# Kernel optimization log

Hardware: AMD Instinct MI355X
Metric: run time of the kernel (lower is better)

## Reference

```python
import jax, jax.numpy as jnp
import numpy as np

B, T1, T2 = 16, 2048, 512
N_MEL, N_TEXT, N_ATT = 80, 256, 256
TEMPERATURE = 0.0005


def _conv1d(x, w, b):
    # x: (B, T, Cin), w: (K, Cin, Cout), 'same' padding
    pad = (w.shape[0] - 1) // 2
    y = jax.lax.conv_general_dilated(
        x, w, window_strides=(1,), padding=[(pad, pad)],
        dimension_numbers=("NWC", "WIO", "NWC"))
    return y + b


def setup_inputs() -> dict:
    key = jax.random.key(0)
    ks = jax.random.split(key, 16)
    s = 0.05
    queries = jax.random.normal(ks[0], (B, N_MEL, T1), jnp.float32)
    keys = jax.random.normal(ks[1], (B, T2, N_TEXT), jnp.float32)
    attn_prior = jax.random.uniform(ks[2], (B, T2, T1), jnp.float32)
    lengths = jax.random.randint(ks[3], (B,), T2 // 2, T2 + 1)
    mask = jnp.arange(T2)[None, :] >= lengths[:, None]  # True = padding
    # key_proj params: Conv(256->512,k3), ReLU, Conv(512->256,k1)
    kw1 = jax.random.normal(ks[4], (3, N_TEXT, 2 * N_TEXT), jnp.float32) * s
    kb1 = jnp.zeros((2 * N_TEXT,), jnp.float32)
    kw2 = jax.random.normal(ks[5], (1, 2 * N_TEXT, N_ATT), jnp.float32) * s
    kb2 = jnp.zeros((N_ATT,), jnp.float32)
    # query_proj params: Conv(80->160,k3), ReLU, Conv(160->80,k1), ReLU, Conv(80->256,k1)
    qw1 = jax.random.normal(ks[6], (3, N_MEL, 2 * N_MEL), jnp.float32) * s
    qb1 = jnp.zeros((2 * N_MEL,), jnp.float32)
    qw2 = jax.random.normal(ks[7], (1, 2 * N_MEL, N_MEL), jnp.float32) * s
    qb2 = jnp.zeros((N_MEL,), jnp.float32)
    qw3 = jax.random.normal(ks[8], (1, N_MEL, N_ATT), jnp.float32) * s
    qb3 = jnp.zeros((N_ATT,), jnp.float32)
    return dict(queries=queries, keys=keys, mask=mask, attn_prior=attn_prior,
                kw1=kw1, kb1=kb1, kw2=kw2, kb2=kb2,
                qw1=qw1, qb1=qb1, qw2=qw2, qb2=qb2, qw3=qw3, qb3=qb3)


def reference(queries, keys, mask, attn_prior,
              kw1, kb1, kw2, kb2, qw1, qb1, qw2, qb2, qw3, qb3):
    # keys: (B, T2, C_text) -> ke: (B, T2, n_att)
    ke = _conv1d(jax.nn.relu(_conv1d(keys, kw1, kb1)), kw2, kb2)
    # queries: (B, C_mel, T1) -> (B, T1, C_mel) -> qe: (B, T1, n_att)
    q = queries.transpose(0, 2, 1)
    q = jax.nn.relu(_conv1d(jax.nn.relu(_conv1d(q, qw1, qb1)), qw2, qb2))
    qe = _conv1d(q, qw3, qb3)
    # pairwise squared L2 distance over channels, via |q|^2 + |k|^2 - 2 q.k
    q2 = jnp.sum(qe * qe, axis=-1)            # (B, T1)
    k2 = jnp.sum(ke * ke, axis=-1)            # (B, T2)
    qk = jnp.einsum("btc,bsc->bts", qe, ke)   # (B, T1, T2)
    dist = q2[:, :, None] + k2[:, None, :] - 2.0 * qk
    attn = (-TEMPERATURE * dist)[:, None]      # (B, 1, T1, T2)
    # prior in log-space
    attn = jax.nn.log_softmax(attn, axis=3) + jnp.log(
        attn_prior.transpose(0, 2, 1)[:, None] + 1e-8)
    attn_logprob = attn
    attn = jnp.where(mask[:, None, None, :], -jnp.inf, attn)
    attn = jax.nn.softmax(attn, axis=3)
    return attn, attn_logprob
```

## Files before the change

### kernel.cpp

```cpp
#include <hip/hip_runtime.h>
#include <cmath>

#define NB    16
#define TT1   2048
#define TT2   512
#define NATT  256
#define TEMP  0.0005f

#define KP_SZ   (NB*514*256)
#define KE_SZ   (NB*512*256)
#define QP_SZ   (NB*2050*80)
#define QE_SZ   (NB*2048*256)
#define W1T_SZ  (512*768)
#define W2T_SZ  (256*512)
#define W3T_SZ  (160*256)
#define W4T_SZ  (80*160)
#define W5T_SZ  (256*96)
#define WTOT_SZ (W1T_SZ+W2T_SZ+W3T_SZ+W4T_SZ+W5T_SZ)
#define LGP_SZ  (NB*TT1*TT2)

#define PREP_PLT_BLK  ((TT1/64)*(TT2/64)*NB)
#define PREP_PK_BLK   (KP_SZ/256)
#define PREP_WT_BLK   (WTOT_SZ/256)
#define PREP_QT_BLK   (NB*(TT1/64))
#define CONV_KEY_BLK  (NB*512/32)
#define CONV_QRY_BLK  (NB*2048/128)

typedef __attribute__((ext_vector_type(8))) short short8v;
typedef __attribute__((ext_vector_type(4))) float f32x4;

__device__ inline ushort f2bf(float f) {
    unsigned int u = __float_as_uint(f);
    u += 0x7fff + ((u >> 16) & 1);
    return (ushort)(u >> 16);
}
__device__ inline float bf2f(ushort u) {
    return __uint_as_float(((unsigned int)u) << 16);
}


__global__ __launch_bounds__(256) void prep_kernel(
    const float* __restrict__ keys, ushort* __restrict__ kp,
    const float* __restrict__ kw1, const float* __restrict__ kw2,
    const float* __restrict__ qw1, const float* __restrict__ qw2,
    const float* __restrict__ qw3,
    ushort* __restrict__ w1t, ushort* __restrict__ w2t, ushort* __restrict__ w3t,
    ushort* __restrict__ w4t, ushort* __restrict__ w5t,
    const float* __restrict__ queries, ushort* __restrict__ qp,
    const float* __restrict__ prior, ushort* __restrict__ lgp)
{
    __shared__ float T[80][65];
    const int bx  = blockIdx.x;
    const int tid = threadIdx.x;

    if (bx < PREP_PLT_BLK) {
        const int l    = bx;
        const int t1_0 = (l & 31) * 64;
        const int t2_0 = ((l >> 5) & 7) * 64;
        const int b    = l >> 8;
        const int j4 = tid & 15;
        const int r0 = tid >> 4;
        #pragma unroll
        for (int p = 0; p < 4; ++p) {
            const f32x4 v = __builtin_nontemporal_load(
                (const f32x4*)(prior + ((size_t)b * TT2 + t2_0 + r0 + p * 16) * TT1
                                + t1_0 + j4 * 4));
            T[r0 + p * 16][j4 * 4 + 0] = v.x;
            T[r0 + p * 16][j4 * 4 + 1] = v.y;
            T[r0 + p * 16][j4 * 4 + 2] = v.z;
            T[r0 + p * 16][j4 * 4 + 3] = v.w;
        }
        __syncthreads();
        const int j  = tid & 63;
        const int i0 = (tid >> 6) * 16;
        #pragma unroll
        for (int r = 0; r < 16; ++r) {
            const int p = i0 + r;
            const float v = T[j][p];
            lgp[((size_t)b * TT1 + t1_0 + p) * TT2 + t2_0 + j] = f2bf(__logf(v + 1e-8f));
        }
        return;
    }
    if (bx < PREP_PLT_BLK + PREP_PK_BLK) {
        const int idx = (bx - PREP_PLT_BLK) * 256 + tid;
        int c = idx & 255;
        int r = (idx >> 8) % 514;
        int b = idx / (514 * 256);
        float v = 0.f;
        if (r >= 1 && r <= 512)
            v = keys[((size_t)b * 512 + (r - 1)) * 256 + c];
        kp[idx] = f2bf(v);
        return;
    }
    if (bx < PREP_PLT_BLK + PREP_PK_BLK + PREP_WT_BLK) {
        int idx = (bx - PREP_PLT_BLK - PREP_PK_BLK) * 256 + tid;
        const float* w; ushort* wt; int Kreal, Kpad, N;
        if (idx < W1T_SZ) {
            w = kw1; wt = w1t; Kreal = 768; Kpad = 768; N = 512;
        } else if ((idx -= W1T_SZ) < W2T_SZ) {
            w = kw2; wt = w2t; Kreal = 512; Kpad = 512; N = 256;
        } else if ((idx -= W2T_SZ) < W3T_SZ) {
            w = qw1; wt = w3t; Kreal = 240; Kpad = 256; N = 160;
        } else if ((idx -= W3T_SZ) < W4T_SZ) {
            w = qw2; wt = w4t; Kreal = 160; Kpad = 160; N = 80;
        } else {
            idx -= W4T_SZ;
            w = qw3; wt = w5t; Kreal = 80; Kpad = 96; N = 256;
        }
        int k = idx % Kpad;
        int n = idx / Kpad;
        wt[idx] = (k < Kreal) ? f2bf(w[(size_t)k * N + n]) : (ushort)0;
        return;
    }
    {
        const int l  = bx - PREP_PLT_BLK - PREP_PK_BLK - PREP_WT_BLK;
        const int b  = l >> 5;
        const int t0 = (l & 31) * 64;
        const int g  = tid >> 6;
        const int j  = tid & 63;
        #pragma unroll
        for (int r = 0; r < 20; ++r) {
            const int c = g * 20 + r;
            T[c][j] = queries[((size_t)b * 80 + c) * 2048 + t0 + j];
        }
        __syncthreads();
        const int tt = tid >> 2;
        const int c0 = (tid & 3) * 20;
        ushort* qrow = qp + (size_t)b * (2050 * 80) + (size_t)(t0 + tt + 1) * 80 + c0;
        #pragma unroll
        for (int i4 = 0; i4 < 5; ++i4) {
            ushort4 st;
            st.x = f2bf(T[c0 + i4 * 4 + 0][tt]);
            st.y = f2bf(T[c0 + i4 * 4 + 1][tt]);
            st.z = f2bf(T[c0 + i4 * 4 + 2][tt]);
            st.w = f2bf(T[c0 + i4 * 4 + 3][tt]);
            *(ushort4*)(qrow + i4 * 4) = st;
        }
        if (t0 == 0 && tid < 80)
            qp[(size_t)b * (2050 * 80) + tid] = 0;
        if (t0 == 2048 - 64 && tid < 80)
            qp[(size_t)b * (2050 * 80) + (size_t)2049 * 80 + tid] = 0;
    }
}


__global__ __launch_bounds__(512, 4) void conv_kernel(
    const ushort* __restrict__ kp, const ushort* __restrict__ w1t,
    const float* __restrict__ kb1, const ushort* __restrict__ w2t,
    const float* __restrict__ kb2, ushort* __restrict__ ke, float* __restrict__ k2,
    const ushort* __restrict__ qp, const ushort* __restrict__ w3t,
    const float* __restrict__ qb1, const ushort* __restrict__ w4t,
    const float* __restrict__ qb2, const ushort* __restrict__ w5t,
    const float* __restrict__ qb3, ushort* __restrict__ qe)
{
    __shared__ __align__(16) unsigned char smem[69632];
    const int bx   = blockIdx.x;
    const int tid  = threadIdx.x;
    const int wv   = tid >> 6;
    const int lane = tid & 63;
    const int lr   = lane & 15;
    const int lk   = lane >> 4;

    if (bx < CONV_KEY_BLK) {
        ushort (*h1s)[536] = (ushort(*)[536])smem;
        float (*k2part)[8] = (float(*)[8])(smem + 32 * 536 * 2);
        const int m0 = bx * 32;

        {
            const ushort* arow0;
            const ushort* arow1;
            {
                const int m = m0 + lr;
                arow0 = kp + (size_t)(m >> 9) * (514 * 256) + (size_t)(m & 511) * 256 + lk * 8;
                const int m1 = m0 + 16 + lr;
                arow1 = kp + (size_t)(m1 >> 9) * (514 * 256) + (size_t)(m1 & 511) * 256 + lk * 8;
            }
            const ushort* wtb = w1t + (size_t)(wv * 64 + lr) * 768 + lk * 8;
            f32x4 acc[2][4];
            #pragma unroll
            for (int mf = 0; mf < 2; ++mf)
                #pragma unroll
                for (int f = 0; f < 4; ++f) acc[mf][f] = (f32x4){0.f, 0.f, 0.f, 0.f};

            short8v a0 = *(const short8v*)(arow0);
            short8v a1 = *(const short8v*)(arow1);
            short8v b0 = *(const short8v*)(wtb);
            short8v b1 = *(const short8v*)(wtb + (size_t)1 * 16 * 768);
            short8v b2 = *(const short8v*)(wtb + (size_t)2 * 16 * 768);
            short8v b3 = *(const short8v*)(wtb + (size_t)3 * 16 * 768);
            #pragma unroll
            for (int ks = 0; ks < 24; ++ks) {
                short8v na0, na1, nb0, nb1, nb2, nb3;
                if (ks < 23) {
                    const int o = (ks + 1) * 32;
                    na0 = *(const short8v*)(arow0 + o);
                    na1 = *(const short8v*)(arow1 + o);
                    nb0 = *(const short8v*)(wtb + o);
                    nb1 = *(const short8v*)(wtb + (size_t)1 * 16 * 768 + o);
                    nb2 = *(const short8v*)(wtb + (size_t)2 * 16 * 768 + o);
                    nb3 = *(const short8v*)(wtb + (size_t)3 * 16 * 768 + o);
                }
                acc[0][0] = __builtin_amdgcn_mfma_f32_16x16x32_bf16(a0, b0, acc[0][0], 0, 0, 0);
                acc[1][0] = __builtin_amdgcn_mfma_f32_16x16x32_bf16(a1, b0, acc[1][0], 0, 0, 0);
                acc[0][1] = __builtin_amdgcn_mfma_f32_16x16x32_bf16(a0, b1, acc[0][1], 0, 0, 0);
                acc[1][1] = __builtin_amdgcn_mfma_f32_16x16x32_bf16(a1, b1, acc[1][1], 0, 0, 0);
                acc[0][2] = __builtin_amdgcn_mfma_f32_16x16x32_bf16(a0, b2, acc[0][2], 0, 0, 0);
                acc[1][2] = __builtin_amdgcn_mfma_f32_16x16x32_bf16(a1, b2, acc[1][2], 0, 0, 0);
                acc[0][3] = __builtin_amdgcn_mfma_f32_16x16x32_bf16(a0, b3, acc[0][3], 0, 0, 0);
                acc[1][3] = __builtin_amdgcn_mfma_f32_16x16x32_bf16(a1, b3, acc[1][3], 0, 0, 0);
                if (ks < 23) {
                    a0 = na0; a1 = na1; b0 = nb0; b1 = nb1; b2 = nb2; b3 = nb3;
                }
            }
            #pragma unroll
            for (int f = 0; f < 4; ++f) {
                const int col = wv * 64 + f * 16 + lr;
                const float bv = kb1[col];
                #pragma unroll
                for (int mf = 0; mf < 2; ++mf)
                    #pragma unroll
                    for (int r = 0; r < 4; ++r)
                        h1s[mf * 16 + lk * 4 + r][col] = f2bf(fmaxf(acc[mf][f][r] + bv, 0.f));
            }
        }
        __syncthreads();

        {
            f32x4 acc[2][2];
            #pragma unroll
            for (int mf = 0; mf < 2; ++mf)
                #pragma unroll
                for (int f = 0; f < 2; ++f) acc[mf][f] = (f32x4){0.f, 0.f, 0.f, 0.f};
            const ushort* w2b = w2t + (size_t)(wv * 32 + lr) * 512 + lk * 8;
            short8v b0 = *(const short8v*)(w2b);
            short8v b1 = *(const short8v*)(w2b + (size_t)16 * 512);
            #pragma unroll
            for (int ks = 0; ks < 16; ++ks) {
                short8v nb0, nb1;
                if (ks < 15) {
                    const int o = (ks + 1) * 32;
                    nb0 = *(const short8v*)(w2b + o);
                    nb1 = *(const short8v*)(w2b + (size_t)16 * 512 + o);
                }
                const short8v a0 = *(const short8v*)&h1s[lr][lk * 8 + ks * 32];
                const short8v a1 = *(const short8v*)&h1s[16 + lr][lk * 8 + ks * 32];
                acc[0][0] = __builtin_amdgcn_mfma_f32_16x16x32_bf16(a0, b0, acc[0][0], 0, 0, 0);
                acc[1][0] = __builtin_amdgcn_mfma_f32_16x16x32_bf16(a1, b0, acc[1][0], 0, 0, 0);
                acc[0][1] = __builtin_amdgcn_mfma_f32_16x16x32_bf16(a0, b1, acc[0][1], 0, 0, 0);
                acc[1][1] = __builtin_amdgcn_mfma_f32_16x16x32_bf16(a1, b1, acc[1][1], 0, 0, 0);
                if (ks < 15) { b0 = nb0; b1 = nb1; }
            }
            float ss[2][4];
            #pragma unroll
            for (int mf = 0; mf < 2; ++mf)
                #pragma unroll
                for (int r = 0; r < 4; ++r) ss[mf][r] = 0.f;
            #pragma unroll
            for (int f = 0; f < 2; ++f) {
                const int col = wv * 32 + f * 16 + lr;
                const float bv = kb2[col];
                #pragma unroll
                for (int mf = 0; mf < 2; ++mf)
                    #pragma unroll
                    for (int r = 0; r < 4; ++r) {
                        const float o = acc[mf][f][r] + bv;
                        ke[(size_t)(m0 + mf * 16 + lk * 4 + r) * 256 + col] = f2bf(o);
                        ss[mf][r] += o * o;
                    }
            }
            #pragma unroll
            for (int mf = 0; mf < 2; ++mf)
                #pragma unroll
                for (int r = 0; r < 4; ++r) {
                    #pragma unroll
                    for (int off = 1; off < 16; off <<= 1)
                        ss[mf][r] += __shfl_xor(ss[mf][r], off);
                }
            if (lr == 0) {
                #pragma unroll
                for (int mf = 0; mf < 2; ++mf)
                    #pragma unroll
                    for (int r = 0; r < 4; ++r)
                        k2part[mf * 16 + lk * 4 + r][wv] = ss[mf][r];
            }
        }
        __syncthreads();
        if (tid < 32) {
            float s = 0.f;
            #pragma unroll
            for (int w = 0; w < 8; ++w) s += k2part[tid][w];
            k2[m0 + tid] = -TEMP * s;
        }
        return;
    }
    {
        ushort (*s1)[168] = (ushort(*)[168])smem;
        ushort (*s2)[104] = (ushort(*)[104])(smem + 128 * 168 * 2);
        const int m0 = (bx - CONV_KEY_BLK) * 128;
        const int cg = wv >> 2;
        const int rb = (wv & 3) * 32;

        #pragma unroll
        for (int i = 0; i < 4; ++i) {
            const int e = tid * 4 + i;
            s2[e >> 4][80 + (e & 15)] = 0;
        }

        {
            const ushort* arow0;
            const ushort* arow1;
            {
                const int m = m0 + rb + lr;
                arow0 = qp + (size_t)(m >> 11) * (2050 * 80) + (size_t)(m & 2047) * 80 + lk * 8;
                const int m1 = m0 + rb + 16 + lr;
                arow1 = qp + (size_t)(m1 >> 11) * (2050 * 80) + (size_t)(m1 & 2047) * 80 + lk * 8;
            }
            const ushort* w3b = w3t + (size_t)(cg * 5 * 16 + lr) * 256 + lk * 8;
            f32x4 acc[2][5];
            #pragma unroll
            for (int mf = 0; mf < 2; ++mf)
                #pragma unroll
                for (int f = 0; f < 5; ++f) acc[mf][f] = (f32x4){0.f, 0.f, 0.f, 0.f};

            short8v a0 = *(const short8v*)(arow0);
            short8v a1 = *(const short8v*)(arow1);
            short8v bq[5];
            #pragma unroll
            for (int f = 0; f < 5; ++f)
                bq[f] = *(const short8v*)(w3b + (size_t)f * 16 * 256);
            #pragma unroll
            for (int ks = 0; ks < 8; ++ks) {
                short8v na0, na1, nb[5];
                if (ks < 7) {
                    const int o = (ks + 1) * 32;
                    na0 = *(const short8v*)(arow0 + o);
                    na1 = *(const short8v*)(arow1 + o);
                    #pragma unroll
                    for (int f = 0; f < 5; ++f)
                        nb[f] = *(const short8v*)(w3b + (size_t)f * 16 * 256 + o);
                }
                #pragma unroll
                for (int f = 0; f < 5; ++f) {
                    acc[0][f] = __builtin_amdgcn_mfma_f32_16x16x32_bf16(a0, bq[f], acc[0][f], 0, 0, 0);
                    acc[1][f] = __builtin_amdgcn_mfma_f32_16x16x32_bf16(a1, bq[f], acc[1][f], 0, 0, 0);
                }
                if (ks < 7) {
                    a0 = na0; a1 = na1;
                    #pragma unroll
                    for (int f = 0; f < 5; ++f) bq[f] = nb[f];
                }
            }
            #pragma unroll
            for (int f = 0; f < 5; ++f) {
                const int col = (cg * 5 + f) * 16 + lr;
                const float bv = qb1[col];
                #pragma unroll
                for (int mf = 0; mf < 2; ++mf)
                    #pragma unroll
                    for (int r = 0; r < 4; ++r)
                        s1[rb + mf * 16 + lk * 4 + r][col] = f2bf(fmaxf(acc[mf][f][r] + bv, 0.f));
            }
        }
        __syncthreads();

        {
            const int nf = cg ? 2 : 3;
            const int f0 = cg ? 3 : 0;
            f32x4 acc[2][3];
            #pragma unroll
            for (int mf = 0; mf < 2; ++mf)
                #pragma unroll
                for (int f = 0; f < 3; ++f) acc[mf][f] = (f32x4){0.f, 0.f, 0.f, 0.f};
            #pragma unroll
            for (int ks = 0; ks < 5; ++ks) {
                const short8v a0 = *(const short8v*)&s1[rb + lr][lk * 8 + ks * 32];
                const short8v a1 = *(const short8v*)&s1[rb + 16 + lr][lk * 8 + ks * 32];
                #pragma unroll
                for (int f = 0; f < 3; ++f) {
                    if (f < nf) {
                        const short8v b = *(const short8v*)(w4t + (size_t)((f0 + f) * 16 + lr) * 160
                                                                + lk * 8 + ks * 32);
                        acc[0][f] = __builtin_amdgcn_mfma_f32_16x16x32_bf16(a0, b, acc[0][f], 0, 0, 0);
                        acc[1][f] = __builtin_amdgcn_mfma_f32_16x16x32_bf16(a1, b, acc[1][f], 0, 0, 0);
                    }
                }
            }
            #pragma unroll
            for (int f = 0; f < 3; ++f) {
                if (f < nf) {
                    const int col = (f0 + f) * 16 + lr;
                    const float bv = qb2[col];
                    #pragma unroll
                    for (int mf = 0; mf < 2; ++mf)
                        #pragma unroll
                        for (int r = 0; r < 4; ++r)
                            s2[rb + mf * 16 + lk * 4 + r][col] = f2bf(fmaxf(acc[mf][f][r] + bv, 0.f));
                }
            }
        }
        __syncthreads();

        {
            f32x4 acc[2][8];
            #pragma unroll
            for (int mf = 0; mf < 2; ++mf)
                #pragma unroll
                for (int f = 0; f < 8; ++f) acc[mf][f] = (f32x4){0.f, 0.f, 0.f, 0.f};
            #pragma unroll
            for (int ks = 0; ks < 3; ++ks) {
                const short8v a0 = *(const short8v*)&s2[rb + lr][lk * 8 + ks * 32];
                const short8v a1 = *(const short8v*)&s2[rb + 16 + lr][lk * 8 + ks * 32];
                #pragma unroll
                for (int f = 0; f < 8; ++f) {
                    const short8v b = *(const short8v*)(w5t + (size_t)((cg * 8 + f) * 16 + lr) * 96
                                                            + lk * 8 + ks * 32);
                    acc[0][f] = __builtin_amdgcn_mfma_f32_16x16x32_bf16(a0, b, acc[0][f], 0, 0, 0);
                    acc[1][f] = __builtin_amdgcn_mfma_f32_16x16x32_bf16(a1, b, acc[1][f], 0, 0, 0);
                }
            }
            #pragma unroll
            for (int f = 0; f < 8; ++f) {
                const int col = (cg * 8 + f) * 16 + lr;
                const float bv = qb3[col];
                #pragma unroll
                for (int mf = 0; mf < 2; ++mf)
                    #pragma unroll
                    for (int r = 0; r < 4; ++r)
                        qe[(size_t)(m0 + rb + mf * 16 + lk * 4 + r) * 256 + col] = f2bf(acc[mf][f][r] + bv);
            }
        }
    }
}


__global__ __launch_bounds__(512) void attn_kernel(
    const ushort* __restrict__ qe, const ushort* __restrict__ ke,
    const float* __restrict__ k2t, const ushort* __restrict__ lgp,
    const unsigned char* __restrict__ mask,
    float* __restrict__ out_attn, float* __restrict__ out_lp)
{
    __shared__ float S[16][516];
    const int b    = blockIdx.x >> 7;
    const int t1_0 = (blockIdx.x & 127) << 4;
    const int tid  = threadIdx.x;
    const int lane = tid & 63;
    const int wv   = tid >> 6;

    {
        const int lr = lane & 15;
        const int lk = lane >> 4;
        const ushort* qrow = qe + ((size_t)b * TT1 + t1_0 + lr) * NATT + lk * 8;
        short8v a[8];
        #pragma unroll
        for (int k = 0; k < 8; ++k)
            a[k] = *(const short8v*)(qrow + k * 32);

        const ushort* kbase = ke + ((size_t)b * TT2 + wv * 64 + lr) * NATT + lk * 8;
        #pragma unroll
        for (int n = 0; n < 4; ++n) {
            f32x4 acc = {0.f, 0.f, 0.f, 0.f};
            const ushort* kb = kbase + (size_t)n * 16 * NATT;
            #pragma unroll
            for (int k = 0; k < 8; ++k) {
                short8v bfr = *(const short8v*)(kb + k * 32);
                acc = __builtin_amdgcn_mfma_f32_16x16x32_bf16(a[k], bfr, acc, 0, 0, 0);
            }
            const int col = wv * 64 + n * 16 + lr;
            const float k2v = k2t[(size_t)b * TT2 + col];
            #pragma unroll
            for (int r = 0; r < 4; ++r)
                S[lk * 4 + r][col] = fmaf(2.0f * TEMP, acc[r], k2v);
        }
    }
    __syncthreads();

    const int rr = tid >> 5;
    const int jj = tid & 31;
    const ushort* lgr = lgp + ((size_t)b * TT1 + t1_0 + rr) * TT2 + jj;
    const unsigned char* mkr = mask + (size_t)b * TT2 + jj;

    float sv[16], uv[16];
    unsigned int mbits = 0;
    #pragma unroll
    for (int k = 0; k < 16; ++k) {
        sv[k] = S[rr][jj + 32 * k];
        uv[k] = sv[k] + bf2f(lgr[32 * k]);
        if (mkr[32 * k]) mbits |= (1u << k);
    }

    float mx1 = sv[0];
    #pragma unroll
    for (int k = 1; k < 16; ++k) mx1 = fmaxf(mx1, sv[k]);
    #pragma unroll
    for (int off = 16; off; off >>= 1) mx1 = fmaxf(mx1, __shfl_xor(mx1, off));
    float se1 = 0.f;
    #pragma unroll
    for (int k = 0; k < 16; ++k) se1 += __expf(sv[k] - mx1);
    #pragma unroll
    for (int off = 16; off; off >>= 1) se1 += __shfl_xor(se1, off);
    const float logZ = mx1 + __logf(se1);

    float mx2 = -INFINITY;
    #pragma unroll
    for (int k = 0; k < 16; ++k)
        if (!((mbits >> k) & 1)) mx2 = fmaxf(mx2, uv[k]);
    #pragma unroll
    for (int off = 16; off; off >>= 1) mx2 = fmaxf(mx2, __shfl_xor(mx2, off));
    float se2 = 0.f;
    #pragma unroll
    for (int k = 0; k < 16; ++k)
        se2 += ((mbits >> k) & 1) ? 0.f : __expf(uv[k] - mx2);
    #pragma unroll
    for (int off = 16; off; off >>= 1) se2 += __shfl_xor(se2, off);
    const float inv = 1.0f / se2;

    float* lpr = out_lp   + ((size_t)b * TT1 + t1_0 + rr) * TT2 + jj;
    float* atr = out_attn + ((size_t)b * TT1 + t1_0 + rr) * TT2 + jj;
    #pragma unroll
    for (int k = 0; k < 16; ++k) {
        lpr[32 * k] = uv[k] - logZ;
        atr[32 * k] = ((mbits >> k) & 1) ? 0.f : __expf(uv[k] - mx2) * inv;
    }
}


extern "C" void kernel_launch(void* const* d_in, const int* in_sizes, int n_in,
                              void* d_out, int out_size, void* d_ws, size_t ws_size,
                              hipStream_t stream) {
    const float* queries = (const float*)d_in[0];
    const float* keys    = (const float*)d_in[1];
    const unsigned char* mask = (const unsigned char*)d_in[2];
    const float* prior   = (const float*)d_in[3];
    const float* kw1 = (const float*)d_in[4];
    const float* kb1 = (const float*)d_in[5];
    const float* kw2 = (const float*)d_in[6];
    const float* kb2 = (const float*)d_in[7];
    const float* qw1 = (const float*)d_in[8];
    const float* qb1 = (const float*)d_in[9];
    const float* qw2 = (const float*)d_in[10];
    const float* qb2 = (const float*)d_in[11];
    const float* qw3 = (const float*)d_in[12];
    const float* qb3 = (const float*)d_in[13];

    ushort* us   = (ushort*)d_ws;
    ushort* kp   = us;
    ushort* ke   = kp  + KP_SZ;
    ushort* qp   = ke  + KE_SZ;
    ushort* qe   = qp  + QP_SZ;
    ushort* w1t  = qe  + QE_SZ;
    ushort* w2t  = w1t + W1T_SZ;
    ushort* w3t  = w2t + W2T_SZ;
    ushort* w4t  = w3t + W3T_SZ;
    ushort* w5t  = w4t + W4T_SZ;
    ushort* lgp  = w5t + W5T_SZ;
    float*  k2   = (float*)(lgp + LGP_SZ);

    float* out_attn = (float*)d_out;
    float* out_lp   = out_attn + (size_t)NB * TT1 * TT2;

    prep_kernel<<<PREP_PLT_BLK + PREP_PK_BLK + PREP_WT_BLK + PREP_QT_BLK, 256, 0, stream>>>(
        keys, kp, kw1, kw2, qw1, qw2, qw3, w1t, w2t, w3t, w4t, w5t,
        queries, qp, prior, lgp);

    conv_kernel<<<CONV_KEY_BLK + CONV_QRY_BLK, 512, 0, stream>>>(
        kp, w1t, kb1, w2t, kb2, ke, k2,
        qp, w3t, qb1, w4t, qb2, w5t, qb3, qe);

    attn_kernel<<<NB * (TT1 / 16), 512, 0, stream>>>(
        qe, ke, k2, lgp, mask, out_attn, out_lp);
}
```

Before: 173.3 us.

## Process 32 query rows per attention block to reuse key fragments

Doubles the query tile per block so each loaded key fragment feeds two MFMA chains, halving key reloads from global/L2. Scores are stored in LDS as bf16 to keep shared memory usage similar, and launch bounds hint 4 blocks per CU. The risk is precision loss in the score values before softmax, plus higher register pressure from holding two query fragment sets.

After: 153.9 us. -11.2%, faster.

```diff
diff --git a/kernel.cpp b/kernel.cpp
--- a/kernel.cpp
+++ b/kernel.cpp
@@ -433,15 +433,15 @@
 }
 
 
-__global__ __launch_bounds__(512) void attn_kernel(
+__global__ __launch_bounds__(512, 4) void attn_kernel(
     const ushort* __restrict__ qe, const ushort* __restrict__ ke,
     const float* __restrict__ k2t, const ushort* __restrict__ lgp,
     const unsigned char* __restrict__ mask,
     float* __restrict__ out_attn, float* __restrict__ out_lp)
 {
-    __shared__ float S[16][516];
-    const int b    = blockIdx.x >> 7;
-    const int t1_0 = (blockIdx.x & 127) << 4;
+    __shared__ ushort S[32][520];
+    const int b    = blockIdx.x >> 6;
+    const int t1_0 = (blockIdx.x & 63) << 5;
     const int tid  = threadIdx.x;
     const int lane = tid & 63;
     const int wv   = tid >> 6;
@@ -449,77 +449,90 @@
     {
         const int lr = lane & 15;
         const int lk = lane >> 4;
-        const ushort* qrow = qe + ((size_t)b * TT1 + t1_0 + lr) * NATT + lk * 8;
-        short8v a[8];
-        #pragma unroll
-        for (int k = 0; k < 8; ++k)
-            a[k] = *(const short8v*)(qrow + k * 32);
+        const ushort* qrow0 = qe + ((size_t)b * TT1 + t1_0 + lr) * NATT + lk * 8;
+        const ushort* qrow1 = qe + ((size_t)b * TT1 + t1_0 + 16 + lr) * NATT + lk * 8;
+        short8v a0[8], a1[8];
+        #pragma unroll
+        for (int k = 0; k < 8; ++k) {
+            a0[k] = *(const short8v*)(qrow0 + k * 32);
+            a1[k] = *(const short8v*)(qrow1 + k * 32);
+        }
 
         const ushort* kbase = ke + ((size_t)b * TT2 + wv * 64 + lr) * NATT + lk * 8;
         #pragma unroll
         for (int n = 0; n < 4; ++n) {
-            f32x4 acc = {0.f, 0.f, 0.f, 0.f};
+            f32x4 acc0 = {0.f, 0.f, 0.f, 0.f};
+            f32x4 acc1 = {0.f, 0.f, 0.f, 0.f};
             const ushort* kb = kbase + (size_t)n * 16 * NATT;
             #pragma unroll
             for (int k = 0; k < 8; ++k) {
-                short8v bfr = *(const short8v*)(kb + k * 32);
-                acc = __builtin_amdgcn_mfma_f32_16x16x32_bf16(a[k], bfr, acc, 0, 0, 0);
+                const short8v bfr = *(const short8v*)(kb + k * 32);
+                acc0 = __builtin_amdgcn_mfma_f32_16x16x32_bf16(a0[k], bfr, acc0, 0, 0, 0);
+                acc1 = __builtin_amdgcn_mfma_f32_16x16x32_bf16(a1[k], bfr, acc1, 0, 0, 0);
             }
             const int col = wv * 64 + n * 16 + lr;
             const float k2v = k2t[(size_t)b * TT2 + col];
             #pragma unroll
-            for (int r = 0; r < 4; ++r)
-                S[lk * 4 + r][col] = fmaf(2.0f * TEMP, acc[r], k2v);
+            for (int r = 0; r < 4; ++r) {
+                S[lk * 4 + r][col]      = f2bf(fmaf(2.0f * TEMP, acc0[r], k2v));
+                S[16 + lk * 4 + r][col] = f2bf(fmaf(2.0f * TEMP, acc1[r], k2v));
+            }
         }
     }
     __syncthreads();
 
-    const int rr = tid >> 5;
     const int jj = tid & 31;
-    const ushort* lgr = lgp + ((size_t)b * TT1 + t1_0 + rr) * TT2 + jj;
     const unsigned char* mkr = mask + (size_t)b * TT2 + jj;
-
-    float sv[16], uv[16];
     unsigned int mbits = 0;
     #pragma unroll
-    for (int k = 0; k < 16; ++k) {
-        sv[k] = S[rr][jj + 32 * k];
-        uv[k] = sv[k] + bf2f(lgr[32 * k]);
+    for (int k = 0; k < 16; ++k)
         if (mkr[32 * k]) mbits |= (1u << k);
-    }
-
-    float mx1 = sv[0];
+
     #pragma unroll
-    for (int k = 1; k < 16; ++k) mx1 = fmaxf(mx1, sv[k]);
-    #pragma unroll
-    for (int off = 16; off; off >>= 1) mx1 = fmaxf(mx1, __shfl_xor(mx1, off));
-    float se1 = 0.f;
-    #pragma unroll
-    for (int k = 0; k < 16; ++k) se1 += __expf(sv[k] - mx1);
-    #pragma unroll
-    for (int off = 16; off; off >>= 1) se1 += __shfl_xor(se1, off);
-    const float logZ = mx1 + __logf(se1);
-
-    float mx2 = -INFINITY;
-    #pragma unroll
-    for (int k = 0; k < 16; ++k)
-        if (!((mbits >> k) & 1)) mx2 = fmaxf(mx2, uv[k]);
-    #pragma unroll
-    for (int off = 16; off; off >>= 1) mx2 = fmaxf(mx2, __shfl_xor(mx2, off));
-    float se2 = 0.f;
-    #pragma unroll
-    for (int k = 0; k < 16; ++k)
-        se2 += ((mbits >> k) & 1) ? 0.f : __expf(uv[k] - mx2);
-    #pragma unroll
-    for (int off = 16; off; off >>= 1) se2 += __shfl_xor(se2, off);
-    const float inv = 1.0f / se2;
-
-    float* lpr = out_lp   + ((size_t)b * TT1 + t1_0 + rr) * TT2 + jj;
-    float* atr = out_attn + ((size_t)b * TT1 + t1_0 + rr) * TT2 + jj;
-    #pragma unroll
-    for (int k = 0; k < 16; ++k) {
-        lpr[32 * k] = uv[k] - logZ;
-        atr[32 * k] = ((mbits >> k) & 1) ? 0.f : __expf(uv[k] - mx2) * inv;
+    for (int half = 0; half < 2; ++half) {
+        const int rr = (tid >> 5) + half * 16;
+        const ushort* lgr = lgp + ((size_t)b * TT1 + t1_0 + rr) * TT2 + jj;
+
+        float sv[16], uv[16];
+        #pragma unroll
+        for (int k = 0; k < 16; ++k) {
+            sv[k] = bf2f(S[rr][jj + 32 * k]);
+            uv[k] = sv[k] + bf2f(lgr[32 * k]);
+        }
+
+        float mx1 = sv[0];
+        #pragma unroll
+        for (int k = 1; k < 16; ++k) mx1 = fmaxf(mx1, sv[k]);
+        #pragma unroll
+        for (int off = 16; off; off >>= 1) mx1 = fmaxf(mx1, __shfl_xor(mx1, off));
+        float se1 = 0.f;
+        #pragma unroll
+        for (int k = 0; k < 16; ++k) se1 += __expf(sv[k] - mx1);
+        #pragma unroll
+        for (int off = 16; off; off >>= 1) se1 += __shfl_xor(se1, off);
+        const float logZ = mx1 + __logf(se1);
+
+        float mx2 = -INFINITY;
+        #pragma unroll
+        for (int k = 0; k < 16; ++k)
+            if (!((mbits >> k) & 1)) mx2 = fmaxf(mx2, uv[k]);
+        #pragma unroll
+        for (int off = 16; off; off >>= 1) mx2 = fmaxf(mx2, __shfl_xor(mx2, off));
+        float se2 = 0.f;
+        #pragma unroll
+        for (int k = 0; k < 16; ++k)
+            se2 += ((mbits >> k) & 1) ? 0.f : __expf(uv[k] - mx2);
+        #pragma unroll
+        for (int off = 16; off; off >>= 1) se2 += __shfl_xor(se2, off);
+        const float inv = 1.0f / se2;
+
+        float* lpr = out_lp   + ((size_t)b * TT1 + t1_0 + rr) * TT2 + jj;
+        float* atr = out_attn + ((size_t)b * TT1 + t1_0 + rr) * TT2 + jj;
+        #pragma unroll
+        for (int k = 0; k < 16; ++k) {
+            lpr[32 * k] = uv[k] - logZ;
+            atr[32 * k] = ((mbits >> k) & 1) ? 0.f : __expf(uv[k] - mx2) * inv;
+        }
     }
 }
 
@@ -566,6 +579,6 @@
         kp, w1t, kb1, w2t, kb2, ke, k2,
         qp, w3t, qb1, w4t, qb2, w5t, qb3, qe);
 
-    attn_kernel<<<NB * (TT1 / 16), 512, 0, stream>>>(
+    attn_kernel<<<NB * (TT1 / 32), 512, 0, stream>>>(
         qe, ke, k2, lgp, mask, out_attn, out_lp);
 }
```
